# Kernel tuning notes

Hardware: AMD Instinct MI355X
Metric: run time of the kernel (lower is better)

## Reference

```python
import jax, jax.numpy as jnp
import numpy as np

TEMPERATURE = 0.01
STRIDE = 16  # original image coords -> feature grid (1024 / 64)


def setup_inputs() -> dict:
    key = jax.random.key(0)
    k1, k2, k3, k4, k5 = jax.random.split(key, 5)
    B, C, Hf, Wf, N = 32, 256, 64, 64, 64
    feats_src = jax.random.normal(k1, (B, C, Hf, Wf), dtype=jnp.float32)
    feats_trg = jax.random.normal(k2, (B, C, Hf, Wf), dtype=jnp.float32)
    # keypoints in original-image coordinates [0, 1024)
    kps_src = jax.random.uniform(k3, (B, N, 2), dtype=jnp.float32) * 1024.0
    kps_trg = jax.random.uniform(k4, (B, N, 2), dtype=jnp.float32) * 1024.0
    kps_mask = jax.random.bernoulli(k5, 0.7, (B, N))
    return {"feats_src": feats_src, "feats_trg": feats_trg,
            "kps_src": kps_src, "kps_trg": kps_trg, "kps_mask": kps_mask}


def _l2_normalize(x):
    # F.normalize(x, dim=1): x / max(||x||_2, eps)
    n = jnp.linalg.norm(x, axis=1, keepdims=True)
    return x / jnp.maximum(n, 1e-12)


def _kps_to_flat_idx(kps, Hf, Wf):
    # int(coord/16) truncation (coords >= 0 so trunc == floor), then clamp.
    fx = jnp.clip((kps[..., 0] / STRIDE).astype(jnp.int32), 0, Wf - 1)
    fy = jnp.clip((kps[..., 1] / STRIDE).astype(jnp.int32), 0, Hf - 1)
    return fy * Wf + fx  # (B, N)


def reference(feats_src, feats_trg, kps_src, kps_trg, kps_mask):
    B, C, Hf, Wf = feats_src.shape
    fs = _l2_normalize(feats_src).reshape(B, C, Hf * Wf)
    ft = _l2_normalize(feats_trg).reshape(B, C, Hf * Wf)

    src_idx = _kps_to_flat_idx(kps_src, Hf, Wf)  # (B, N)
    trg_idx = _kps_to_flat_idx(kps_trg, Hf, Wf)  # (B, N)

    # Gather query vectors at source keypoint cells: (B, C, N)
    queries = jnp.take_along_axis(fs, src_idx[:, None, :], axis=2)
    # Batched logits over all target cells: (B, N, Hf*Wf)
    logits = jnp.einsum('bcn,bcm->bnm', queries, ft) / TEMPERATURE

    logp = jax.nn.log_softmax(logits, axis=-1)
    nll = -jnp.take_along_axis(logp, trg_idx[..., None], axis=-1)[..., 0]  # (B, N)

    m = kps_mask.astype(nll.dtype)
    count = jnp.sum(m)
    # Masked mean over valid keypoints; 0 if no valid keypoints (matches torch).
    return jnp.sum(nll * m) / jnp.maximum(count, 1.0)
```

## Files before the change

kernel.cpp:

```cpp
#include <hip/hip_runtime.h>
#include <hip/hip_fp16.h>
#include <cstdint>

#define BB 32
#define CC 256
#define HF 64
#define WF 64
#define MM 4096
#define NN 64
#define MCHUNKS 32
#define MPB 128
#define KSTEPS 8

typedef _Float16 half8 __attribute__((ext_vector_type(8)));
typedef float f32x4 __attribute__((ext_vector_type(4)));


__global__ void phase0_gather_norm(const float* __restrict__ fs,
                                   const float* __restrict__ kps_src,
                                   const float* __restrict__ kps_trg,
                                   _Float16* __restrict__ wq,
                                   int* __restrict__ trgidx) {
  int blk = blockIdx.x;
  int b = blk >> 6, n = blk & 63;
  int c = threadIdx.x;

  float kx = kps_src[blk * 2 + 0];
  float ky = kps_src[blk * 2 + 1];
  int fx = min(max((int)(kx * (1.0f / 16.0f)), 0), WF - 1);
  int fy = min(max((int)(ky * (1.0f / 16.0f)), 0), HF - 1);
  int pix = fy * WF + fx;

  float x = fs[((size_t)b * CC + c) * MM + pix];

  float v = x * x;
  #pragma unroll
  for (int off = 32; off >= 1; off >>= 1) v += __shfl_xor(v, off);
  __shared__ float ssum[4];
  int wid = c >> 6, lane = c & 63;
  if (lane == 0) ssum[wid] = v;
  __syncthreads();
  float tot = ssum[0] + ssum[1] + ssum[2] + ssum[3];
  float inv = 1.0f / fmaxf(sqrtf(tot), 1e-12f);

  int ks = c >> 5, kg = (c >> 3) & 3, j = c & 7;
  int nt = n >> 4, nr = n & 15;
  int lane_f = kg * 16 + nr;
  size_t off = (size_t)b * 16384 + (size_t)((ks * 4 + nt) * 64 + lane_f) * 8 + j;
  wq[off] = (_Float16)(x * inv);

  if (c == 0) {
    float tx = kps_trg[blk * 2 + 0], ty = kps_trg[blk * 2 + 1];
    int gx = min(max((int)(tx * (1.0f / 16.0f)), 0), WF - 1);
    int gy = min(max((int)(ty * (1.0f / 16.0f)), 0), HF - 1);
    trgidx[blk] = gy * WF + gx;
  }
}

__global__ void __launch_bounds__(256, 4)
phaseB(const float* __restrict__ ft,
       const _Float16* __restrict__ wq,
       const int* __restrict__ tidx,
       float* __restrict__ part,
       float* __restrict__ trgl) {
  __shared__ _Float16 qf[16384];
  __shared__ int trg_lds[NN];
  __shared__ float pM[4 * NN], pS[4 * NN];

  int b = blockIdx.x >> 5, mc = blockIdx.x & 31;
  int tid = threadIdx.x;

  const uint4* src = (const uint4*)(wq + (size_t)b * 16384);
  uint4* dst = (uint4*)qf;
  #pragma unroll
  for (int i = 0; i < 8; ++i) dst[tid + 256 * i] = src[tid + 256 * i];
  if (tid < NN) trg_lds[tid] = tidx[b * NN + tid];
  __syncthreads();

  int w = tid >> 6, lane = tid & 63, g = lane >> 4, col = lane & 15;
  int m0 = mc * MPB + w * 32;
  const float* fb = ft + (size_t)b * CC * MM;
  const float* lb0 = fb + (size_t)(g * 8) * MM + (m0 + col);
  const float* lb1 = lb0 + 16;

  f32x4 acc[4][2];
  #pragma unroll
  for (int nt = 0; nt < 4; ++nt)
    #pragma unroll
    for (int mt = 0; mt < 2; ++mt) acc[nt][mt] = (f32x4){0.f, 0.f, 0.f, 0.f};
  float ss0 = 0.f, ss1 = 0.f;

  const half8* qv = (const half8*)qf;
  for (int ks = 0; ks < KSTEPS; ++ks) {
    half8 a0 = qv[(ks * 4 + 0) * 64 + lane];
    half8 a1 = qv[(ks * 4 + 1) * 64 + lane];
    half8 a2 = qv[(ks * 4 + 2) * 64 + lane];
    half8 a3 = qv[(ks * 4 + 3) * 64 + lane];

    float f0[8], f1[8];
    #pragma unroll
    for (int j = 0; j < 8; ++j) f0[j] = lb0[(size_t)(ks * 32 + j) * MM];
    #pragma unroll
    for (int j = 0; j < 8; ++j) f1[j] = lb1[(size_t)(ks * 32 + j) * MM];

    half8 b0, b1;
    #pragma unroll
    for (int j = 0; j < 8; ++j) {
      ss0 += f0[j] * f0[j];
      ss1 += f1[j] * f1[j];
      b0[j] = (_Float16)f0[j];
      b1[j] = (_Float16)f1[j];
    }

    acc[0][0] = __builtin_amdgcn_mfma_f32_16x16x32_f16(a0, b0, acc[0][0], 0, 0, 0);
    acc[1][0] = __builtin_amdgcn_mfma_f32_16x16x32_f16(a1, b0, acc[1][0], 0, 0, 0);
    acc[2][0] = __builtin_amdgcn_mfma_f32_16x16x32_f16(a2, b0, acc[2][0], 0, 0, 0);
    acc[3][0] = __builtin_amdgcn_mfma_f32_16x16x32_f16(a3, b0, acc[3][0], 0, 0, 0);
    acc[0][1] = __builtin_amdgcn_mfma_f32_16x16x32_f16(a0, b1, acc[0][1], 0, 0, 0);
    acc[1][1] = __builtin_amdgcn_mfma_f32_16x16x32_f16(a1, b1, acc[1][1], 0, 0, 0);
    acc[2][1] = __builtin_amdgcn_mfma_f32_16x16x32_f16(a2, b1, acc[2][1], 0, 0, 0);
    acc[3][1] = __builtin_amdgcn_mfma_f32_16x16x32_f16(a3, b1, acc[3][1], 0, 0, 0);
  }

  ss0 += __shfl_xor(ss0, 16); ss0 += __shfl_xor(ss0, 32);
  ss1 += __shfl_xor(ss1, 16); ss1 += __shfl_xor(ss1, 32);
  float scale0 = 100.0f / fmaxf(sqrtf(ss0), 1e-12f);
  float scale1 = 100.0f / fmaxf(sqrtf(ss1), 1e-12f);

  int mA = m0 + col, mB = m0 + 16 + col;

  #pragma unroll
  for (int nt = 0; nt < 4; ++nt) {
    #pragma unroll
    for (int r = 0; r < 4; ++r) {
      int n = nt * 16 + g * 4 + r;
      float v0 = acc[nt][0][r] * scale0;
      float v1 = acc[nt][1][r] * scale1;
      int t = trg_lds[n];
      if (t == mA) trgl[b * NN + n] = v0;
      if (t == mB) trgl[b * NN + n] = v1;
      float mx = fmaxf(v0, v1);
      #pragma unroll
      for (int off = 8; off >= 1; off >>= 1) mx = fmaxf(mx, __shfl_xor(mx, off));
      float s = __expf(v0 - mx) + __expf(v1 - mx);
      #pragma unroll
      for (int off = 8; off >= 1; off >>= 1) s += __shfl_xor(s, off);
      if (col == 0) { pM[w * NN + n] = mx; pS[w * NN + n] = s; }
    }
  }
  __syncthreads();

  if (tid < NN) {
    int n = tid;
    float gm = fmaxf(fmaxf(pM[n], pM[NN + n]), fmaxf(pM[2 * NN + n], pM[3 * NN + n]));
    float S = 0.f;
    #pragma unroll
    for (int ww = 0; ww < 4; ++ww)
      S += pS[ww * NN + n] * __expf(pM[ww * NN + n] - gm);
    size_t o = ((size_t)(b * MCHUNKS + mc) * NN + n) * 2;
    part[o] = gm;
    part[o + 1] = S;
  }
}

__global__ void reduceA(const float* __restrict__ part,
                        const float* __restrict__ trgl,
                        float* __restrict__ nll) {
  int p = blockIdx.x * 256 + threadIdx.x;
  int b = p >> 6, n = p & 63;
  float gm = -1e30f;
  #pragma unroll
  for (int mc = 0; mc < MCHUNKS; ++mc)
    gm = fmaxf(gm, part[((size_t)(b * MCHUNKS + mc) * NN + n) * 2]);
  float S = 0.f;
  #pragma unroll
  for (int mc = 0; mc < MCHUNKS; ++mc) {
    size_t o = ((size_t)(b * MCHUNKS + mc) * NN + n) * 2;
    S += part[o + 1] * __expf(part[o] - gm);
  }
  nll[p] = gm + logf(S) - trgl[p];
}

__global__ void reduceB(const float* __restrict__ nll,
                        const void* __restrict__ maskp,
                        float* __restrict__ out) {
  int tid = threadIdx.x;
  __shared__ int flagF, flagB;
  if (tid == 0) { flagF = 0; flagB = 0; }
  __syncthreads();

  const unsigned char* mb = (const unsigned char*)maskp;
  int lf = 0, lb = 0;
  for (int i = tid; i < BB * NN; i += 256) {
    unsigned char v = mb[i];
    int r = i & 3;
    if (r == 3 && v == 0x3F) lf = 1;
    if (r != 0 && v != 0) lb = 1;
  }
  if (lf) atomicOr(&flagF, 1);
  if (lb) atomicOr(&flagB, 1);
  __syncthreads();
  int layout = flagF ? 2 : (flagB ? 0 : 1);

  float lsum = 0.f, lcnt = 0.f;
  for (int p = tid; p < BB * NN; p += 256) {
    float mval;
    if (layout == 2) mval = ((const float*)maskp)[p];
    else if (layout == 0) mval = (float)mb[p];
    else mval = (float)((const int*)maskp)[p];
    lsum += nll[p] * mval;
    lcnt += mval;
  }

  #pragma unroll
  for (int off = 32; off >= 1; off >>= 1) {
    lsum += __shfl_xor(lsum, off);
    lcnt += __shfl_xor(lcnt, off);
  }
  __shared__ float sS[4], sC[4];
  int wid = tid >> 6, lane = tid & 63;
  if (lane == 0) { sS[wid] = lsum; sC[wid] = lcnt; }
  __syncthreads();
  if (tid == 0) {
    float s = sS[0] + sS[1] + sS[2] + sS[3];
    float cn = sC[0] + sC[1] + sC[2] + sC[3];
    out[0] = s / fmaxf(cn, 1.0f);
  }
}

extern "C" void kernel_launch(void* const* d_in, const int* in_sizes, int n_in,
                              void* d_out, int out_size, void* d_ws, size_t ws_size,
                              hipStream_t stream) {
  const float* fs   = (const float*)d_in[0];
  const float* ft   = (const float*)d_in[1];
  const float* ksrc = (const float*)d_in[2];
  const float* ktrg = (const float*)d_in[3];
  const void*  mask = d_in[4];
  float* out = (float*)d_out;

  _Float16* wq = (_Float16*)d_ws;
  float* part  = (float*)((char*)d_ws + (size_t)BB * 16384 * 2);
  float* trgl  = part + (size_t)BB * MCHUNKS * NN * 2;
  float* nll   = trgl + BB * NN;
  int* tidx    = (int*)(nll + BB * NN);

  phase0_gather_norm<<<BB * NN, 256, 0, stream>>>(fs, ksrc, ktrg, wq, tidx);
  phaseB<<<BB * MCHUNKS, 256, 0, stream>>>(ft, wq, tidx, part, trgl);
  reduceA<<<BB * NN / 256, 256, 0, stream>>>(part, trgl, nll);
  reduceB<<<1, 256, 0, stream>>>(nll, mask, out);
}
```

Before: 55.45 us.

## Prefetch next k-step features in phaseB and fuse both reductions into one kernel

The main kernel now software-pipelines its global feature loads, issuing the next k-step's loads before the current step's MFMAs, and uses packed fp16 conversion. The two final reduction kernels are merged into a single 1024-thread block that reduces the partial log-sum-exp and applies the mask. The partial buffer is relaid out chunk-major so those reads coalesce. This removes one kernel launch and the nll round trip through memory, at the cost of higher register pressure in phaseB and a single-block reduction.

```diff
diff --git a/kernel.cpp b/kernel.cpp
--- a/kernel.cpp
+++ b/kernel.cpp
@@ -13,6 +13,7 @@
 #define KSTEPS 8
 
 typedef _Float16 half8 __attribute__((ext_vector_type(8)));
+typedef __fp16 fp16x2 __attribute__((ext_vector_type(2)));
 typedef float f32x4 __attribute__((ext_vector_type(4)));
 
 
@@ -91,25 +92,38 @@
   float ss0 = 0.f, ss1 = 0.f;
 
   const half8* qv = (const half8*)qf;
+
+  float cur0[8], cur1[8], nxt0[8], nxt1[8];
+  #pragma unroll
+  for (int j = 0; j < 8; ++j) {
+    cur0[j] = lb0[(size_t)j * MM];
+    cur1[j] = lb1[(size_t)j * MM];
+  }
+
+  #pragma unroll
   for (int ks = 0; ks < KSTEPS; ++ks) {
+    if (ks + 1 < KSTEPS) {
+      #pragma unroll
+      for (int j = 0; j < 8; ++j) {
+        nxt0[j] = lb0[(size_t)((ks + 1) * 32 + j) * MM];
+        nxt1[j] = lb1[(size_t)((ks + 1) * 32 + j) * MM];
+      }
+    }
+
     half8 a0 = qv[(ks * 4 + 0) * 64 + lane];
     half8 a1 = qv[(ks * 4 + 1) * 64 + lane];
     half8 a2 = qv[(ks * 4 + 2) * 64 + lane];
     half8 a3 = qv[(ks * 4 + 3) * 64 + lane];
 
-    float f0[8], f1[8];
-    #pragma unroll
-    for (int j = 0; j < 8; ++j) f0[j] = lb0[(size_t)(ks * 32 + j) * MM];
-    #pragma unroll
-    for (int j = 0; j < 8; ++j) f1[j] = lb1[(size_t)(ks * 32 + j) * MM];
-
     half8 b0, b1;
     #pragma unroll
-    for (int j = 0; j < 8; ++j) {
-      ss0 += f0[j] * f0[j];
-      ss1 += f1[j] * f1[j];
-      b0[j] = (_Float16)f0[j];
-      b1[j] = (_Float16)f1[j];
+    for (int j = 0; j < 4; ++j) {
+      ss0 += cur0[2 * j] * cur0[2 * j] + cur0[2 * j + 1] * cur0[2 * j + 1];
+      ss1 += cur1[2 * j] * cur1[2 * j] + cur1[2 * j + 1] * cur1[2 * j + 1];
+      fp16x2 h0 = __builtin_amdgcn_cvt_pkrtz(cur0[2 * j], cur0[2 * j + 1]);
+      fp16x2 h1 = __builtin_amdgcn_cvt_pkrtz(cur1[2 * j], cur1[2 * j + 1]);
+      b0[2 * j] = (_Float16)h0[0]; b0[2 * j + 1] = (_Float16)h0[1];
+      b1[2 * j] = (_Float16)h1[0]; b1[2 * j + 1] = (_Float16)h1[1];
     }
 
     acc[0][0] = __builtin_amdgcn_mfma_f32_16x16x32_f16(a0, b0, acc[0][0], 0, 0, 0);
@@ -120,6 +134,9 @@
     acc[1][1] = __builtin_amdgcn_mfma_f32_16x16x32_f16(a1, b1, acc[1][1], 0, 0, 0);
     acc[2][1] = __builtin_amdgcn_mfma_f32_16x16x32_f16(a2, b1, acc[2][1], 0, 0, 0);
     acc[3][1] = __builtin_amdgcn_mfma_f32_16x16x32_f16(a3, b1, acc[3][1], 0, 0, 0);
+
+    #pragma unroll
+    for (int j = 0; j < 8; ++j) { cur0[j] = nxt0[j]; cur1[j] = nxt1[j]; }
   }
 
   ss0 += __shfl_xor(ss0, 16); ss0 += __shfl_xor(ss0, 32);
@@ -157,41 +174,26 @@
     #pragma unroll
     for (int ww = 0; ww < 4; ++ww)
       S += pS[ww * NN + n] * __expf(pM[ww * NN + n] - gm);
-    size_t o = ((size_t)(b * MCHUNKS + mc) * NN + n) * 2;
+    size_t o = ((size_t)mc * (BB * NN) + b * NN + n) * 2;
     part[o] = gm;
     part[o + 1] = S;
   }
 }
 
-__global__ void reduceA(const float* __restrict__ part,
-                        const float* __restrict__ trgl,
-                        float* __restrict__ nll) {
-  int p = blockIdx.x * 256 + threadIdx.x;
-  int b = p >> 6, n = p & 63;
-  float gm = -1e30f;
-  #pragma unroll
-  for (int mc = 0; mc < MCHUNKS; ++mc)
-    gm = fmaxf(gm, part[((size_t)(b * MCHUNKS + mc) * NN + n) * 2]);
-  float S = 0.f;
-  #pragma unroll
-  for (int mc = 0; mc < MCHUNKS; ++mc) {
-    size_t o = ((size_t)(b * MCHUNKS + mc) * NN + n) * 2;
-    S += part[o + 1] * __expf(part[o] - gm);
-  }
-  nll[p] = gm + logf(S) - trgl[p];
-}
-
-__global__ void reduceB(const float* __restrict__ nll,
-                        const void* __restrict__ maskp,
-                        float* __restrict__ out) {
+__global__ void __launch_bounds__(1024)
+reduceAB(const float* __restrict__ part,
+         const float* __restrict__ trgl,
+         const void* __restrict__ maskp,
+         float* __restrict__ out) {
   int tid = threadIdx.x;
+
   __shared__ int flagF, flagB;
   if (tid == 0) { flagF = 0; flagB = 0; }
   __syncthreads();
 
   const unsigned char* mb = (const unsigned char*)maskp;
   int lf = 0, lb = 0;
-  for (int i = tid; i < BB * NN; i += 256) {
+  for (int i = tid; i < BB * NN; i += 1024) {
     unsigned char v = mb[i];
     int r = i & 3;
     if (r == 3 && v == 0x3F) lf = 1;
@@ -203,12 +205,26 @@
   int layout = flagF ? 2 : (flagB ? 0 : 1);
 
   float lsum = 0.f, lcnt = 0.f;
-  for (int p = tid; p < BB * NN; p += 256) {
+  #pragma unroll
+  for (int h = 0; h < 2; ++h) {
+    int p = tid + h * 1024;
+    float gm = -1e30f;
+    #pragma unroll
+    for (int c = 0; c < MCHUNKS; ++c)
+      gm = fmaxf(gm, part[((size_t)c * (BB * NN) + p) * 2]);
+    float S = 0.f;
+    #pragma unroll
+    for (int c = 0; c < MCHUNKS; ++c) {
+      size_t o = ((size_t)c * (BB * NN) + p) * 2;
+      S += part[o + 1] * __expf(part[o] - gm);
+    }
+    float nll = gm + logf(S) - trgl[p];
+
     float mval;
     if (layout == 2) mval = ((const float*)maskp)[p];
     else if (layout == 0) mval = (float)mb[p];
     else mval = (float)((const int*)maskp)[p];
-    lsum += nll[p] * mval;
+    lsum += nll * mval;
     lcnt += mval;
   }
 
@@ -217,13 +233,14 @@
     lsum += __shfl_xor(lsum, off);
     lcnt += __shfl_xor(lcnt, off);
   }
-  __shared__ float sS[4], sC[4];
+  __shared__ float sS[16], sC[16];
   int wid = tid >> 6, lane = tid & 63;
   if (lane == 0) { sS[wid] = lsum; sC[wid] = lcnt; }
   __syncthreads();
   if (tid == 0) {
-    float s = sS[0] + sS[1] + sS[2] + sS[3];
-    float cn = sC[0] + sC[1] + sC[2] + sC[3];
+    float s = 0.f, cn = 0.f;
+    #pragma unroll
+    for (int i = 0; i < 16; ++i) { s += sS[i]; cn += sC[i]; }
     out[0] = s / fmaxf(cn, 1.0f);
   }
 }
@@ -240,12 +257,10 @@
 
   _Float16* wq = (_Float16*)d_ws;
   float* part  = (float*)((char*)d_ws + (size_t)BB * 16384 * 2);
-  float* trgl  = part + (size_t)BB * MCHUNKS * NN * 2;
-  float* nll   = trgl + BB * NN;
-  int* tidx    = (int*)(nll + BB * NN);
+  float* trgl  = part + (size_t)MCHUNKS * BB * NN * 2;
+  int* tidx    = (int*)(trgl + BB * NN);
 
   phase0_gather_norm<<<BB * NN, 256, 0, stream>>>(fs, ksrc, ktrg, wq, tidx);
   phaseB<<<BB * MCHUNKS, 256, 0, stream>>>(ft, wq, tidx, part, trgl);
-  reduceA<<<BB * NN / 256, 256, 0, stream>>>(part, trgl, nll);
-  reduceB<<<1, 256, 0, stream>>>(nll, mask, out);
-}
+  reduceAB<<<1, 1024, 0, stream>>>(part, trgl, mask, out);
+}
```

Result: slower. 58.08 us (+4.7%).
